# Kernel optimization log

Measured on AMD Instinct MI355X. Metric: run time of the kernel, lower is better.

## Reference

```python
import jax, jax.numpy as jnp
import numpy as np

N0, N1, N2 = 200000, 600000, 400000
NNZ1, NNZ2 = 1200000, 1200000
G = 256          # number of graphs in the batch
H = 128          # num_hidden
NIN = 32         # num_input
L = 2            # num_layers
R = 3            # max_rank + 1


def setup_inputs() -> dict:
    key = jax.random.key(0)
    ks = jax.random.split(key, 24)
    d = {}
    d["x0"] = jax.random.normal(ks[0], (N0, NIN), jnp.float32)
    d["x1"] = jax.random.normal(ks[1], (N1, NIN), jnp.float32)
    d["x2"] = jax.random.normal(ks[2], (N2, NIN), jnp.float32)
    d["b1_rows"] = jax.random.randint(ks[3], (NNZ1,), 0, N0, jnp.int32)
    d["b1_cols"] = jax.random.randint(ks[4], (NNZ1,), 0, N1, jnp.int32)
    d["b2_rows"] = jax.random.randint(ks[5], (NNZ2,), 0, N1, jnp.int32)
    d["b2_cols"] = jax.random.randint(ks[6], (NNZ2,), 0, N2, jnp.int32)
    d["batch0"] = jnp.sort(jax.random.randint(ks[7], (N0,), 0, G, jnp.int32))
    d["batch1"] = jnp.sort(jax.random.randint(ks[8], (N1,), 0, G, jnp.int32))
    d["batch2"] = jnp.sort(jax.random.randint(ks[9], (N2,), 0, G, jnp.int32))
    sin = 1.0 / np.sqrt(NIN).astype(np.float32)
    sh = 1.0 / np.sqrt(H).astype(np.float32)
    d["w_emb"] = jax.random.normal(ks[10], (NIN, H), jnp.float32) * sin
    d["b_emb"] = jnp.zeros((H,), jnp.float32)
    # one conv weight per (layer, rank>0): message W for B_r^T @ (x @ W)
    d["conv_w"] = jax.random.normal(ks[11], (L, 2, H, H), jnp.float32) * sh
    d["pre_w1"] = jax.random.normal(ks[12], (R, H, H), jnp.float32) * sh
    d["pre_b1"] = jnp.zeros((R, H), jnp.float32)
    d["pre_w2"] = jax.random.normal(ks[13], (R, H, H), jnp.float32) * sh
    d["pre_b2"] = jnp.zeros((R, H), jnp.float32)
    d["post_w1"] = jax.random.normal(ks[14], (R * H, H), jnp.float32) * (1.0 / np.sqrt(R * H).astype(np.float32))
    d["post_b1"] = jnp.zeros((H,), jnp.float32)
    d["post_w2"] = jax.random.normal(ks[15], (H, 1), jnp.float32) * sh
    d["post_b2"] = jnp.zeros((1,), jnp.float32)
    return d


def reference(x0, x1, x2, b1_rows, b1_cols, b2_rows, b2_cols,
              batch0, batch1, batch2,
              w_emb, b_emb, conv_w,
              pre_w1, pre_b1, pre_w2, pre_b2,
              post_w1, post_b1, post_w2, post_b2):
    # feature embedding (shared across ranks)
    h0 = x0 @ w_emb + b_emb
    h1 = x1 @ w_emb + b_emb
    h2 = x2 @ w_emb + b_emb

    for l in range(L):
        # sparse incidence matmul B_r^T @ h_{r-1}: gather rows, scatter-add to cols
        m1 = jax.ops.segment_sum(h0[b1_rows], b1_cols, num_segments=N1)
        m2 = jax.ops.segment_sum(h1[b2_rows], b2_cols, num_segments=N2)
        # aggregation with sigmoid update; rank 0 has no incoming messages
        h0 = jax.nn.sigmoid(h0)
        h1 = jax.nn.sigmoid(m1 @ conv_w[l, 0])
        h2 = jax.nn.sigmoid(m2 @ conv_w[l, 1])

    def pre_pool(h, r):
        z = jax.nn.silu(h @ pre_w1[r] + pre_b1[r])
        return z @ pre_w2[r] + pre_b2[r]

    # global_add_pool per rank -> [G, H] each
    p0 = jax.ops.segment_sum(pre_pool(h0, 0), batch0, num_segments=G)
    p1 = jax.ops.segment_sum(pre_pool(h1, 1), batch1, num_segments=G)
    p2 = jax.ops.segment_sum(pre_pool(h2, 2), batch2, num_segments=G)

    state = jnp.concatenate([p0, p1, p2], axis=1)  # [G, 3H]
    z = jax.nn.silu(state @ post_w1 + post_b1)
    out = z @ post_w2 + post_b2                     # [G, 1]
    return jnp.squeeze(out, axis=-1)                # [G]
```

## Files before the change

kernel.cpp:

```cpp
#include <hip/hip_runtime.h>
#include <math.h>

#define HDIM 128
#define NIN_ 32
#define RANKS 3

typedef unsigned int u32;
typedef unsigned short u16;
typedef __attribute__((ext_vector_type(8))) short short8;
typedef __attribute__((ext_vector_type(8))) __bf16 bf16x8;
typedef __attribute__((ext_vector_type(4))) float f32x4;

__device__ __forceinline__ u16 f2bf(float f) { return __builtin_bit_cast(u16, (__bf16)f); }
__device__ __forceinline__ float bf2f(u16 b) { return (float)__builtin_bit_cast(__bf16, b); }

__device__ __forceinline__ float sigmoidf_(float x) {
    return __builtin_amdgcn_rcpf(1.0f + __builtin_amdgcn_exp2f(-1.44269504f * x));
}
__device__ __forceinline__ float siluf_(float x) { return x * sigmoidf_(x); }

template <int SIG>
__device__ __forceinline__ float sigpow(float f) {
#pragma unroll
    for (int q = 0; q < SIG; ++q) f = sigmoidf_(f);
    return f;
}

__global__ void zero_kernel(u32* __restrict__ p, long long nw) {
    long long i = (long long)blockIdx.x * blockDim.x + threadIdx.x;
    long long stride = (long long)gridDim.x * blockDim.x;
    for (; i < nw; i += stride) p[i] = 0u;
}

__global__ void count2_kernel(const int* __restrict__ c1, int n1, int* __restrict__ cntA,
                              const int* __restrict__ c2, int n2, int* __restrict__ cntB) {
    int e = blockIdx.x * 256 + threadIdx.x;
    if (e < n1) atomicAdd(&cntA[c1[e]], 1);
    else if (e < n1 + n2) atomicAdd(&cntB[c2[e - n1]], 1);
}

__global__ void fill2_kernel(const int* __restrict__ r1, const int* __restrict__ c1,
                             int* __restrict__ curA, int* __restrict__ esrc1, int n1,
                             const int* __restrict__ r2, const int* __restrict__ c2,
                             int* __restrict__ curB, int* __restrict__ esrc2, int n2) {
    int e = blockIdx.x * 256 + threadIdx.x;
    if (e < n1) {
        int i = atomicAdd(&curA[c1[e]], 1);
        esrc1[i] = r1[e];
    } else if (e < n1 + n2) {
        int ee = e - n1;
        int i = atomicAdd(&curB[c2[ee]], 1);
        esrc2[i] = r2[ee];
    }
}

__global__ void scan1_kernel(const int* __restrict__ cnt, int* __restrict__ bsum, int ndst) {
    __shared__ int lds[256];
    int base = blockIdx.x * 1024, t = threadIdx.x;
    int s = 0;
#pragma unroll
    for (int j = 0; j < 4; ++j) {
        int i = base + t * 4 + j;
        s += (i < ndst) ? cnt[i] : 0;
    }
    lds[t] = s;
    __syncthreads();
    for (int off = 128; off > 0; off >>= 1) {
        if (t < off) lds[t] += lds[t + off];
        __syncthreads();
    }
    if (t == 0) bsum[blockIdx.x] = lds[0];
}

__global__ void scan2_kernel(int* __restrict__ bsum, int nb, int* __restrict__ total) {
    __shared__ int lds[256];
    int t = threadIdx.x;
    int v[8];
    int s = 0;
#pragma unroll
    for (int j = 0; j < 8; ++j) {
        int i = t * 8 + j;
        v[j] = (i < nb) ? bsum[i] : 0;
        s += v[j];
    }
    lds[t] = s;
    __syncthreads();
    for (int off = 1; off < 256; off <<= 1) {
        int y = (t >= off) ? lds[t - off] : 0;
        __syncthreads();
        lds[t] += y;
        __syncthreads();
    }
    int run = lds[t] - s;
#pragma unroll
    for (int j = 0; j < 8; ++j) {
        int i = t * 8 + j;
        if (i < nb) {
            bsum[i] = run;
            run += v[j];
        }
    }
    if (t == 255) *total = run;
}

__global__ void scan3_kernel(const int* __restrict__ cnt, const int* __restrict__ bsum,
                             int* __restrict__ rowptr, int* __restrict__ cursor, int ndst) {
    __shared__ int lds[256];
    int base = blockIdx.x * 1024, t = threadIdx.x;
    int v[4];
    int s = 0;
#pragma unroll
    for (int j = 0; j < 4; ++j) {
        int i = base + t * 4 + j;
        v[j] = (i < ndst) ? cnt[i] : 0;
        s += v[j];
    }
    lds[t] = s;
    __syncthreads();
    for (int off = 1; off < 256; off <<= 1) {
        int y = (t >= off) ? lds[t - off] : 0;
        __syncthreads();
        lds[t] += y;
        __syncthreads();
    }
    int run = bsum[blockIdx.x] + lds[t] - s;
#pragma unroll
    for (int j = 0; j < 4; ++j) {
        int i = base + t * 4 + j;
        if (i < ndst) {
            rowptr[i] = run;
            cursor[i] = run;
            run += v[j];
        }
    }
}

__global__ void wprep_kernel(const float* __restrict__ conv_w, const float* __restrict__ pre_w1,
                             const float* __restrict__ pre_w2, u16* __restrict__ wt, int Lnum) {
    int tid = blockIdx.x * 256 + threadIdx.x;
    int nm = 2 * Lnum + 6;
    if (tid >= nm * 128 * 128) return;
    int m = tid >> 14;
    int r = tid & 16383;
    int k = r >> 7;
    int col = r & 127;
    const float* src;
    if (m < 2 * Lnum) src = conv_w + (size_t)m * 16384;
    else if (m < 2 * Lnum + 3) src = pre_w1 + (size_t)(m - 2 * Lnum) * 16384;
    else src = pre_w2 + (size_t)(m - 2 * Lnum - 3) * 16384;
    float v = src[k * 128 + col];
    wt[(size_t)m * 16384 + col * 128 + (k ^ ((col & 7) << 3))] = f2bf(v);
}

__global__ void wembprep_kernel(const float* __restrict__ w_emb, u16* __restrict__ wembT) {
    int tid = blockIdx.x * 256 + threadIdx.x;
    if (tid >= HDIM * NIN_) return;
    int col = tid >> 5, k = tid & 31;
    wembT[col * 32 + k] = f2bf(w_emb[k * HDIM + col]);
}

__global__ __launch_bounds__(512) void embed_mfma_kernel(const float* __restrict__ x,
                                                         const u16* __restrict__ wembT,
                                                         const float* __restrict__ b,
                                                         u16* __restrict__ h, int n) {
    __shared__ u16 cs[8][16][128];
    const int tid = threadIdx.x;
    const int wave = tid >> 6, lane = tid & 63;
    const int row0 = blockIdx.x * 128;
    const int col = lane & 15, kg = lane >> 4;
    const int wrow0 = row0 + wave * 16;
    const int arow = wrow0 + col;
    const int arowc = arow < n ? arow : (n - 1);

    bf16x8 afrag;
    {
        const float4* xp = (const float4*)(x + (size_t)arowc * NIN_ + kg * 8);
        float4 xa = xp[0], xb = xp[1];
        short8 s;
        s[0] = (short)f2bf(xa.x); s[1] = (short)f2bf(xa.y);
        s[2] = (short)f2bf(xa.z); s[3] = (short)f2bf(xa.w);
        s[4] = (short)f2bf(xb.x); s[5] = (short)f2bf(xb.y);
        s[6] = (short)f2bf(xb.z); s[7] = (short)f2bf(xb.w);
        afrag = __builtin_bit_cast(bf16x8, s);
    }

#pragma unroll
    for (int ct = 0; ct < 8; ++ct) {
        int bcol = ct * 16 + col;
        bf16x8 bfrag = *(const bf16x8*)(wembT + bcol * 32 + kg * 8);
        f32x4 acc = (f32x4){0.f, 0.f, 0.f, 0.f};
        acc = __builtin_amdgcn_mfma_f32_16x16x32_bf16(afrag, bfrag, acc, 0, 0, 0);
        float bv = b[bcol];
#pragma unroll
        for (int r = 0; r < 4; ++r) {
            int crow = kg * 4 + r;
            cs[wave][crow][(ct * 16 + col) ^ ((crow & 7) << 3)] = f2bf(acc[r] + bv);
        }
    }
#pragma unroll
    for (int it = 0; it < 4; ++it) {
        int cid = it * 64 + lane;
        int r = cid >> 4, c = cid & 15;
        int grow = wrow0 + r;
        if (grow < n) {
            short8 v = *(const short8*)(&cs[wave][r][(c * 8) ^ ((r & 7) << 3)]);
            *(short8*)(h + (size_t)grow * HDIM + c * 8) = v;
        }
    }
}

__device__ __forceinline__ void gemm128(const bf16x8 afrag[4], const u16* wls, f32x4 acc[8],
                                        int col, int kg) {
#pragma unroll
    for (int ct = 0; ct < 8; ++ct) {
        int bcol = ct * 16 + col;
        const u16* bb = wls + bcol * 128;
        int swz = (bcol & 7) << 3;
#pragma unroll
        for (int k0 = 0; k0 < 4; ++k0) {
            bf16x8 bfrag = *(const bf16x8*)(bb + ((k0 * 32 + kg * 8) ^ swz));
            acc[ct] = __builtin_amdgcn_mfma_f32_16x16x32_bf16(afrag[k0], bfrag, acc[ct], 0, 0, 0);
        }
    }
}

__device__ __forceinline__ void stage_w(const u16* __restrict__ w, u16* wls, int tid) {
    const uint4* g = (const uint4*)w;
    uint4* l = (uint4*)wls;
#pragma unroll
    for (int i = 0; i < 4; ++i) l[tid + i * 512] = g[tid + i * 512];
}

__device__ __forceinline__ void pool_acc(const f32x4 acc[8], const float* __restrict__ b2,
                                         const int* __restrict__ batch, float* __restrict__ p,
                                         int n, int colOff, int wrow0, int col, int kg) {
    if (wrow0 >= n) return;
    int rend = wrow0 + 15 < n ? wrow0 + 15 : (n - 1);
    int bstart = batch[wrow0];
    int bend = batch[rend];
    if (bstart == bend) {
#pragma unroll
        for (int ct = 0; ct < 8; ++ct) {
            float b2v = b2[ct * 16 + col];
            float s = 0.f;
#pragma unroll
            for (int r = 0; r < 4; ++r) {
                int row = wrow0 + kg * 4 + r;
                if (row < n) s += acc[ct][r] + b2v;
            }
            s += __shfl_xor(s, 16, 64);
            s += __shfl_xor(s, 32, 64);
            if (kg == 0) atomicAdd(&p[bstart * (RANKS * HDIM) + colOff + ct * 16 + col], s);
        }
    } else {
        int bgs[4];
#pragma unroll
        for (int r = 0; r < 4; ++r) {
            int row = wrow0 + kg * 4 + r;
            bgs[r] = (row < n) ? batch[row] : -1;
        }
#pragma unroll
        for (int ct = 0; ct < 8; ++ct) {
            float b2v = b2[ct * 16 + col];
            int curb = -1;
            float cur = 0.f;
#pragma unroll
            for (int r = 0; r < 4; ++r) {
                if (bgs[r] >= 0) {
                    if (bgs[r] != curb) {
                        if (curb >= 0)
                            atomicAdd(&p[curb * (RANKS * HDIM) + colOff + ct * 16 + col], cur);
                        curb = bgs[r];
                        cur = 0.f;
                    }
                    cur += acc[ct][r] + b2v;
                }
            }
            if (curb >= 0) atomicAdd(&p[curb * (RANKS * HDIM) + colOff + ct * 16 + col], cur);
        }
    }
}

template <int SIGA>
__global__ __launch_bounds__(512) void merged_n1_kernel(
    const u16* __restrict__ srcbuf, const int* __restrict__ rowptr,
    const int* __restrict__ esrc, const u16* __restrict__ wc0, const u16* __restrict__ wc1,
    const u16* __restrict__ w1t, const u16* __restrict__ w2t,
    const float* __restrict__ b1, const float* __restrict__ b2,
    const int* __restrict__ batch, float* __restrict__ p, int colOff,
    u16* __restrict__ outB, int n) {
    __shared__ u16 wls[16384];
    __shared__ u16 zs[8][16][128];
    const int tid = threadIdx.x;
    const int wave = tid >> 6, lane = tid & 63;
    const int row0 = blockIdx.x * 128;
    const int col = lane & 15, kg = lane >> 4;
    const int wrow0 = row0 + wave * 16;

    stage_w(wc0, wls, tid);

    float gr[4][8], gs[4][8];
#pragma unroll
    for (int k0 = 0; k0 < 4; ++k0)
#pragma unroll
        for (int j = 0; j < 8; ++j) { gr[k0][j] = 0.f; gs[k0][j] = 0.f; }

    const int arow = wrow0 + col;
    if (arow < n) {
        int beg = rowptr[arow], end = rowptr[arow + 1];
        for (int e = beg; e < end; e += 2) {
            int s0 = esrc[e];
            bool has1 = (e + 1 < end);
            int s1 = has1 ? esrc[e + 1] : s0;
            const bf16x8* p0 = (const bf16x8*)(srcbuf + (size_t)s0 * HDIM + kg * 8);
            const bf16x8* p1 = (const bf16x8*)(srcbuf + (size_t)s1 * HDIM + kg * 8);
            bf16x8 v0[4], v1[4];
#pragma unroll
            for (int k0 = 0; k0 < 4; ++k0) { v0[k0] = p0[k0 * 4]; v1[k0] = p1[k0 * 4]; }
#pragma unroll
            for (int k0 = 0; k0 < 4; ++k0) {
                short8 sv = __builtin_bit_cast(short8, v0[k0]);
#pragma unroll
                for (int j = 0; j < 8; ++j) {
                    float f = sigpow<SIGA>(bf2f((u16)sv[j]));
                    gr[k0][j] += f;
                    gs[k0][j] += sigmoidf_(f);
                }
            }
            if (has1) {
#pragma unroll
                for (int k0 = 0; k0 < 4; ++k0) {
                    short8 sv = __builtin_bit_cast(short8, v1[k0]);
#pragma unroll
                    for (int j = 0; j < 8; ++j) {
                        float f = sigpow<SIGA>(bf2f((u16)sv[j]));
                        gr[k0][j] += f;
                        gs[k0][j] += sigmoidf_(f);
                    }
                }
            }
        }
    }
    bf16x8 afragR[4], afragS[4];
#pragma unroll
    for (int k0 = 0; k0 < 4; ++k0) {
        short8 sR, sS;
#pragma unroll
        for (int j = 0; j < 8; ++j) {
            sR[j] = (short)f2bf(gr[k0][j]);
            sS[j] = (short)f2bf(gs[k0][j]);
        }
        afragR[k0] = __builtin_bit_cast(bf16x8, sR);
        afragS[k0] = __builtin_bit_cast(bf16x8, sS);
    }
    __syncthreads();

    f32x4 acc[8];
#pragma unroll
    for (int ct = 0; ct < 8; ++ct) acc[ct] = (f32x4){0.f, 0.f, 0.f, 0.f};
    gemm128(afragR, wls, acc, col, kg);
#pragma unroll
    for (int ct = 0; ct < 8; ++ct)
#pragma unroll
        for (int r = 0; r < 4; ++r) {
            int crow = kg * 4 + r;
            zs[wave][crow][(ct * 16 + col) ^ ((crow & 7) << 3)] = f2bf(sigmoidf_(acc[ct][r]));
        }
#pragma unroll
    for (int it = 0; it < 4; ++it) {
        int cid = it * 64 + lane;
        int r = cid >> 4, c = cid & 15;
        int grow = wrow0 + r;
        if (grow < n) {
            short8 v = *(const short8*)(&zs[wave][r][(c * 8) ^ ((r & 7) << 3)]);
            *(short8*)(outB + (size_t)grow * HDIM + c * 8) = v;
        }
    }

    __syncthreads();
    stage_w(wc1, wls, tid);
    __syncthreads();

#pragma unroll
    for (int ct = 0; ct < 8; ++ct) acc[ct] = (f32x4){0.f, 0.f, 0.f, 0.f};
    gemm128(afragS, wls, acc, col, kg);
#pragma unroll
    for (int ct = 0; ct < 8; ++ct)
#pragma unroll
        for (int r = 0; r < 4; ++r) {
            int crow = kg * 4 + r;
            zs[wave][crow][(ct * 16 + col) ^ ((crow & 7) << 3)] = f2bf(sigmoidf_(acc[ct][r]));
        }
    __syncthreads();
    stage_w(w1t, wls, tid);
    __syncthreads();

    bf16x8 zfrag[4];
    {
        int zswz = (col & 7) << 3;
#pragma unroll
        for (int k0 = 0; k0 < 4; ++k0)
            zfrag[k0] = *(const bf16x8*)(&zs[wave][col][(k0 * 32 + kg * 8) ^ zswz]);
    }
#pragma unroll
    for (int ct = 0; ct < 8; ++ct) acc[ct] = (f32x4){0.f, 0.f, 0.f, 0.f};
    gemm128(zfrag, wls, acc, col, kg);
#pragma unroll
    for (int ct = 0; ct < 8; ++ct) {
        float b1v = b1[ct * 16 + col];
#pragma unroll
        for (int r = 0; r < 4; ++r) {
            int crow = kg * 4 + r;
            zs[wave][crow][(ct * 16 + col) ^ ((crow & 7) << 3)] = f2bf(siluf_(acc[ct][r] + b1v));
        }
    }
    __syncthreads();
    stage_w(w2t, wls, tid);
    __syncthreads();

    {
        int zswz = (col & 7) << 3;
#pragma unroll
        for (int k0 = 0; k0 < 4; ++k0)
            zfrag[k0] = *(const bf16x8*)(&zs[wave][col][(k0 * 32 + kg * 8) ^ zswz]);
    }
#pragma unroll
    for (int ct = 0; ct < 8; ++ct) acc[ct] = (f32x4){0.f, 0.f, 0.f, 0.f};
    gemm128(zfrag, wls, acc, col, kg);

    pool_acc(acc, b2, batch, p, n, colOff, wrow0, col, kg);
}

template <int MODE, int SIG>
__global__ __launch_bounds__(512) void fused_mfma_kernel(
    const u16* __restrict__ srcbuf, const int* __restrict__ rowptr,
    const int* __restrict__ esrc, const u16* __restrict__ wconv,
    const u16* __restrict__ w1t, const u16* __restrict__ w2t,
    const float* __restrict__ b1, const float* __restrict__ b2,
    const int* __restrict__ batch, float* __restrict__ p, int colOff,
    u16* __restrict__ outB, int n) {
    __shared__ u16 wls[16384];
    __shared__ u16 zs[8][16][128];
    const int tid = threadIdx.x;
    const int wave = tid >> 6, lane = tid & 63;
    const int row0 = blockIdx.x * 128;
    const int col = lane & 15, kg = lane >> 4;
    const int wrow0 = row0 + wave * 16;

    stage_w(wconv, wls, tid);

    float ga[4][8];
#pragma unroll
    for (int k0 = 0; k0 < 4; ++k0)
#pragma unroll
        for (int j = 0; j < 8; ++j) ga[k0][j] = 0.f;
    const int arow = wrow0 + col;
    if (arow < n) {
        int beg = rowptr[arow], end = rowptr[arow + 1];
        for (int e = beg; e < end; e += 2) {
            int s0 = esrc[e];
            bool has1 = (e + 1 < end);
            int s1 = has1 ? esrc[e + 1] : s0;
            const bf16x8* p0 = (const bf16x8*)(srcbuf + (size_t)s0 * HDIM + kg * 8);
            const bf16x8* p1 = (const bf16x8*)(srcbuf + (size_t)s1 * HDIM + kg * 8);
            bf16x8 v0[4], v1[4];
#pragma unroll
            for (int k0 = 0; k0 < 4; ++k0) { v0[k0] = p0[k0 * 4]; v1[k0] = p1[k0 * 4]; }
#pragma unroll
            for (int k0 = 0; k0 < 4; ++k0) {
                short8 sv = __builtin_bit_cast(short8, v0[k0]);
#pragma unroll
                for (int j = 0; j < 8; ++j) ga[k0][j] += sigpow<SIG>(bf2f((u16)sv[j]));
            }
            if (has1) {
#pragma unroll
                for (int k0 = 0; k0 < 4; ++k0) {
                    short8 sv = __builtin_bit_cast(short8, v1[k0]);
#pragma unroll
                    for (int j = 0; j < 8; ++j) ga[k0][j] += sigpow<SIG>(bf2f((u16)sv[j]));
                }
            }
        }
    }
    bf16x8 afrag[4];
#pragma unroll
    for (int k0 = 0; k0 < 4; ++k0) {
        short8 s;
#pragma unroll
        for (int j = 0; j < 8; ++j) s[j] = (short)f2bf(ga[k0][j]);
        afrag[k0] = __builtin_bit_cast(bf16x8, s);
    }
    __syncthreads();

    f32x4 acc[8];
#pragma unroll
    for (int ct = 0; ct < 8; ++ct) acc[ct] = (f32x4){0.f, 0.f, 0.f, 0.f};
    gemm128(afrag, wls, acc, col, kg);

#pragma unroll
    for (int ct = 0; ct < 8; ++ct)
#pragma unroll
        for (int r = 0; r < 4; ++r) {
            int crow = kg * 4 + r;
            zs[wave][crow][(ct * 16 + col) ^ ((crow & 7) << 3)] = f2bf(sigmoidf_(acc[ct][r]));
        }

    if (MODE == 0) {
#pragma unroll
        for (int it = 0; it < 4; ++it) {
            int cid = it * 64 + lane;
            int r = cid >> 4, c = cid & 15;
            int grow = wrow0 + r;
            if (grow < n) {
                short8 v = *(const short8*)(&zs[wave][r][(c * 8) ^ ((r & 7) << 3)]);
                *(short8*)(outB + (size_t)grow * HDIM + c * 8) = v;
            }
        }
        return;
    }

    __syncthreads();
    stage_w(w1t, wls, tid);
    __syncthreads();

    bf16x8 zfrag[4];
    {
        int zswz = (col & 7) << 3;
#pragma unroll
        for (int k0 = 0; k0 < 4; ++k0)
            zfrag[k0] = *(const bf16x8*)(&zs[wave][col][(k0 * 32 + kg * 8) ^ zswz]);
    }
#pragma unroll
    for (int ct = 0; ct < 8; ++ct) acc[ct] = (f32x4){0.f, 0.f, 0.f, 0.f};
    gemm128(zfrag, wls, acc, col, kg);
#pragma unroll
    for (int ct = 0; ct < 8; ++ct) {
        float b1v = b1[ct * 16 + col];
#pragma unroll
        for (int r = 0; r < 4; ++r) {
            int crow = kg * 4 + r;
            zs[wave][crow][(ct * 16 + col) ^ ((crow & 7) << 3)] = f2bf(siluf_(acc[ct][r] + b1v));
        }
    }
    __syncthreads();
    stage_w(w2t, wls, tid);
    __syncthreads();

    {
        int zswz = (col & 7) << 3;
#pragma unroll
        for (int k0 = 0; k0 < 4; ++k0)
            zfrag[k0] = *(const bf16x8*)(&zs[wave][col][(k0 * 32 + kg * 8) ^ zswz]);
    }
#pragma unroll
    for (int ct = 0; ct < 8; ++ct) acc[ct] = (f32x4){0.f, 0.f, 0.f, 0.f};
    gemm128(zfrag, wls, acc, col, kg);

    pool_acc(acc, b2, batch, p, n, colOff, wrow0, col, kg);
}

template <int SIG>
__global__ __launch_bounds__(512) void prepool_mfma_kernel(
    const u16* __restrict__ h, const u16* __restrict__ w1t, const u16* __restrict__ w2t,
    const float* __restrict__ b1, const float* __restrict__ b2, const int* __restrict__ batch,
    float* __restrict__ p, int n, int colOff) {
    __shared__ u16 wls[16384];
    __shared__ u16 zs[8][16][128];
    const int tid = threadIdx.x;
    const int wave = tid >> 6, lane = tid & 63;
    const int row0 = blockIdx.x * 128;
    const int col = lane & 15, kg = lane >> 4;
    const int wrow0 = row0 + wave * 16;

    stage_w(w1t, wls, tid);

    const int arow = wrow0 + col;
    const int arowc = arow < n ? arow : (n - 1);
    bf16x8 afrag[4];
    {
        const bf16x8* ap = (const bf16x8*)(h + (size_t)arowc * HDIM + kg * 8);
#pragma unroll
        for (int k0 = 0; k0 < 4; ++k0) afrag[k0] = ap[k0 * 4];
    }
    if (SIG > 0) {
#pragma unroll
        for (int k0 = 0; k0 < 4; ++k0) {
            short8 s = __builtin_bit_cast(short8, afrag[k0]);
#pragma unroll
            for (int j = 0; j < 8; ++j) s[j] = (short)f2bf(sigpow<SIG>(bf2f((u16)s[j])));
            afrag[k0] = __builtin_bit_cast(bf16x8, s);
        }
    }
    __syncthreads();

    f32x4 acc[8];
#pragma unroll
    for (int ct = 0; ct < 8; ++ct) acc[ct] = (f32x4){0.f, 0.f, 0.f, 0.f};
    gemm128(afrag, wls, acc, col, kg);
#pragma unroll
    for (int ct = 0; ct < 8; ++ct) {
        float b1v = b1[ct * 16 + col];
#pragma unroll
        for (int r = 0; r < 4; ++r) {
            int crow = kg * 4 + r;
            zs[wave][crow][(ct * 16 + col) ^ ((crow & 7) << 3)] = f2bf(siluf_(acc[ct][r] + b1v));
        }
    }
    __syncthreads();
    stage_w(w2t, wls, tid);
    __syncthreads();

    bf16x8 zfrag[4];
    {
        int zswz = (col & 7) << 3;
#pragma unroll
        for (int k0 = 0; k0 < 4; ++k0)
            zfrag[k0] = *(const bf16x8*)(&zs[wave][col][(k0 * 32 + kg * 8) ^ zswz]);
    }
#pragma unroll
    for (int ct = 0; ct < 8; ++ct) acc[ct] = (f32x4){0.f, 0.f, 0.f, 0.f};
    gemm128(zfrag, wls, acc, col, kg);

    pool_acc(acc, b2, batch, p, n, colOff, wrow0, col, kg);
}

__global__ void final_kernel(const float* __restrict__ p, const float* __restrict__ w1,
                             const float* __restrict__ b1, const float* __restrict__ w2,
                             const float* __restrict__ b2, float* __restrict__ out) {
    const int g = blockIdx.x;
    const int c = threadIdx.x;
    const float* pg = p + g * (RANKS * HDIM);
    float acc = b1[c];
    for (int k = 0; k < RANKS * HDIM; ++k) acc = fmaf(pg[k], w1[k * HDIM + c], acc);
    float z = siluf_(acc);
    float v = z * w2[c];
#pragma unroll
    for (int off = 32; off > 0; off >>= 1) v += __shfl_down(v, off, 64);
    __shared__ float red[2];
    if ((c & 63) == 0) red[c >> 6] = v;
    __syncthreads();
    if (c == 0) out[g] = red[0] + red[1] + b2[0];
}

extern "C" void kernel_launch(void* const* d_in, const int* in_sizes, int n_in,
                              void* d_out, int out_size, void* d_ws, size_t ws_size,
                              hipStream_t stream) {
    const float* x0 = (const float*)d_in[0];
    const float* x1 = (const float*)d_in[1];
    const int* b1_rows = (const int*)d_in[3];
    const int* b1_cols = (const int*)d_in[4];
    const int* b2_rows = (const int*)d_in[5];
    const int* b2_cols = (const int*)d_in[6];
    const int* batch0 = (const int*)d_in[7];
    const int* batch1 = (const int*)d_in[8];
    const int* batch2 = (const int*)d_in[9];
    const float* w_emb = (const float*)d_in[10];
    const float* b_emb = (const float*)d_in[11];
    const float* conv_w = (const float*)d_in[12];
    const float* pre_w1 = (const float*)d_in[13];
    const float* pre_b1 = (const float*)d_in[14];
    const float* pre_w2 = (const float*)d_in[15];
    const float* pre_b2 = (const float*)d_in[16];
    const float* post_w1 = (const float*)d_in[17];
    const float* post_b1 = (const float*)d_in[18];
    const float* post_w2 = (const float*)d_in[19];
    const float* post_b2 = (const float*)d_in[20];

    const int N0 = in_sizes[0] / NIN_;
    const int N1 = in_sizes[1] / NIN_;
    const int N2 = in_sizes[2] / NIN_;
    const int NNZ1 = in_sizes[3];
    const int NNZ2 = in_sizes[5];
    const int L = in_sizes[12] / (2 * HDIM * HDIM);
    const int Gn = out_size;

    u16* A = (u16*)d_ws;
    u16* B = A + (size_t)N0 * HDIM;
    float* p = (float*)(B + (size_t)N1 * HDIM);
    u16* wt = (u16*)(p + (size_t)Gn * RANKS * HDIM);
    const u16* wt_conv = wt;
    const u16* wt_p1 = wt + (size_t)2 * L * 16384;
    const u16* wt_p2 = wt_p1 + (size_t)3 * 16384;
    u16* wembT = wt + (size_t)(2 * L + 6) * 16384;
    int* ip = (int*)(wembT + 4096);
    int* rowptr1 = ip;  ip += N1 + 1;
    int* rowptr2 = ip;  ip += N2 + 1;
    int* esrc1 = ip;    ip += NNZ1;
    int* esrc2 = ip;    ip += NNZ2;
    int* cntA = ip;     ip += N1;
    int* cntB = ip;     ip += N2;
    int* curA = ip;     ip += N1;
    int* curB = ip;     ip += N2;
    int* bsum = ip;     ip += 2048;

    {
        int tot = (2 * L + 6) * 16384;
        wprep_kernel<<<(tot + 255) / 256, 256, 0, stream>>>(conv_w, pre_w1, pre_w2, wt, L);
        wembprep_kernel<<<16, 256, 0, stream>>>(w_emb, wembT);

        zero_kernel<<<1024, 256, 0, stream>>>((u32*)cntA, (long long)(N1 + N2));
        count2_kernel<<<(NNZ1 + NNZ2 + 255) / 256, 256, 0, stream>>>(b1_cols, NNZ1, cntA,
                                                                     b2_cols, NNZ2, cntB);
        int nb1 = (N1 + 1023) / 1024;
        scan1_kernel<<<nb1, 256, 0, stream>>>(cntA, bsum, N1);
        scan2_kernel<<<1, 256, 0, stream>>>(bsum, nb1, rowptr1 + N1);
        scan3_kernel<<<nb1, 256, 0, stream>>>(cntA, bsum, rowptr1, curA, N1);
        int nb2 = (N2 + 1023) / 1024;
        scan1_kernel<<<nb2, 256, 0, stream>>>(cntB, bsum, N2);
        scan2_kernel<<<1, 256, 0, stream>>>(bsum, nb2, rowptr2 + N2);
        scan3_kernel<<<nb2, 256, 0, stream>>>(cntB, bsum, rowptr2, curB, N2);
        fill2_kernel<<<(NNZ1 + NNZ2 + 255) / 256, 256, 0, stream>>>(
            b1_rows, b1_cols, curA, esrc1, NNZ1, b2_rows, b2_cols, curB, esrc2, NNZ2);
    }

    embed_mfma_kernel<<<(N0 + 127) / 128, 512, 0, stream>>>(x0, wembT, b_emb, A, N0);

    zero_kernel<<<64, 256, 0, stream>>>((u32*)p, (long long)Gn * RANKS * HDIM);

    if (L >= 2) {
        int grid = (N1 + 127) / 128;
        const u16* wc0 = wt_conv + (size_t)((L - 2) * 2 + 0) * 16384;
        const u16* wc1 = wt_conv + (size_t)((L - 1) * 2 + 0) * 16384;
        switch (L - 2) {
            case 0: merged_n1_kernel<0><<<grid, 512, 0, stream>>>(
                        A, rowptr1, esrc1, wc0, wc1, wt_p1 + 16384, wt_p2 + 16384,
                        pre_b1 + HDIM, pre_b2 + HDIM, batch1, p, HDIM, B, N1); break;
            case 1: merged_n1_kernel<1><<<grid, 512, 0, stream>>>(
                        A, rowptr1, esrc1, wc0, wc1, wt_p1 + 16384, wt_p2 + 16384,
                        pre_b1 + HDIM, pre_b2 + HDIM, batch1, p, HDIM, B, N1); break;
            default: merged_n1_kernel<2><<<grid, 512, 0, stream>>>(
                        A, rowptr1, esrc1, wc0, wc1, wt_p1 + 16384, wt_p2 + 16384,
                        pre_b1 + HDIM, pre_b2 + HDIM, batch1, p, HDIM, B, N1); break;
        }
    } else {
        embed_mfma_kernel<<<(N1 + 127) / 128, 512, 0, stream>>>(x1, wembT, b_emb, B, N1);
        fused_mfma_kernel<1, 0><<<(N1 + 127) / 128, 512, 0, stream>>>(
            A, rowptr1, esrc1, wt_conv, wt_p1 + 16384, wt_p2 + 16384,
            pre_b1 + HDIM, pre_b2 + HDIM, batch1, p, HDIM, nullptr, N1);
    }

    fused_mfma_kernel<1, 0><<<(N2 + 127) / 128, 512, 0, stream>>>(
        B, rowptr2, esrc2, wt_conv + (size_t)((L - 1) * 2 + 1) * 16384,
        wt_p1 + 2 * 16384, wt_p2 + 2 * 16384, pre_b1 + 2 * HDIM, pre_b2 + 2 * HDIM,
        batch2, p, 2 * HDIM, nullptr, N2);

    {
        int grid = (N0 + 127) / 128;
        switch (L) {
            case 1: prepool_mfma_kernel<1><<<grid, 512, 0, stream>>>(
                        A, wt_p1, wt_p2, pre_b1, pre_b2, batch0, p, N0, 0); break;
            case 2: prepool_mfma_kernel<2><<<grid, 512, 0, stream>>>(
                        A, wt_p1, wt_p2, pre_b1, pre_b2, batch0, p, N0, 0); break;
            default: prepool_mfma_kernel<3><<<grid, 512, 0, stream>>>(
                        A, wt_p1, wt_p2, pre_b1, pre_b2, batch0, p, N0, 0); break;
        }
    }

    final_kernel<<<Gn, HDIM, 0, stream>>>(p, post_w1, post_b1, post_w2, post_b2, (float*)d_out);
}
```

Baseline: 905.1 us.

## Read GEMM weights directly from global memory instead of staging in LDS

Removes the per-block LDS staging of 128x128 bf16 weight matrices and the barriers around it. The MFMA B fragments are now loaded straight from global or L2 memory, and the XOR swizzle is dropped from the weight layout. This cuts LDS use, which may raise occupancy, and removes the syncthreads stalls between GEMM stages. In exchange, every wave re-reads the weights through the cache hierarchy. The bf16 conversions are also replaced with manual bit-manipulation round-to-nearest-even code.

```diff
diff --git a/kernel.cpp b/kernel.cpp
--- a/kernel.cpp
+++ b/kernel.cpp
@@ -11,9 +11,12 @@
 typedef __attribute__((ext_vector_type(8))) __bf16 bf16x8;
 typedef __attribute__((ext_vector_type(4))) float f32x4;
 
-__device__ __forceinline__ u16 f2bf(float f) { return __builtin_bit_cast(u16, (__bf16)f); }
-__device__ __forceinline__ float bf2f(u16 b) { return (float)__builtin_bit_cast(__bf16, b); }
-
+__device__ __forceinline__ float bf2f(u16 b) { return __uint_as_float(((u32)b) << 16); }
+__device__ __forceinline__ u16 f2bf(float f) {
+    u32 u = __float_as_uint(f);
+    u32 r = u + 0x7fffu + ((u >> 16) & 1u);
+    return (u16)(r >> 16);
+}
 __device__ __forceinline__ float sigmoidf_(float x) {
     return __builtin_amdgcn_rcpf(1.0f + __builtin_amdgcn_exp2f(-1.44269504f * x));
 }
@@ -149,7 +152,7 @@
     else if (m < 2 * Lnum + 3) src = pre_w1 + (size_t)(m - 2 * Lnum) * 16384;
     else src = pre_w2 + (size_t)(m - 2 * Lnum - 3) * 16384;
     float v = src[k * 128 + col];
-    wt[(size_t)m * 16384 + col * 128 + (k ^ ((col & 7) << 3))] = f2bf(v);
+    wt[(size_t)m * 16384 + col * 128 + k] = f2bf(v);
 }
 
 __global__ void wembprep_kernel(const float* __restrict__ w_emb, u16* __restrict__ wembT) {
@@ -209,26 +212,18 @@
     }
 }
 
-__device__ __forceinline__ void gemm128(const bf16x8 afrag[4], const u16* wls, f32x4 acc[8],
-                                        int col, int kg) {
+__device__ __forceinline__ void gemm128g(const bf16x8 afrag[4], const u16* __restrict__ wt,
+                                         f32x4 acc[8], int col, int kg) {
 #pragma unroll
     for (int ct = 0; ct < 8; ++ct) {
         int bcol = ct * 16 + col;
-        const u16* bb = wls + bcol * 128;
-        int swz = (bcol & 7) << 3;
+        const u16* bb = wt + bcol * 128 + kg * 8;
 #pragma unroll
         for (int k0 = 0; k0 < 4; ++k0) {
-            bf16x8 bfrag = *(const bf16x8*)(bb + ((k0 * 32 + kg * 8) ^ swz));
+            bf16x8 bfrag = *(const bf16x8*)(bb + k0 * 32);
             acc[ct] = __builtin_amdgcn_mfma_f32_16x16x32_bf16(afrag[k0], bfrag, acc[ct], 0, 0, 0);
         }
     }
-}
-
-__device__ __forceinline__ void stage_w(const u16* __restrict__ w, u16* wls, int tid) {
-    const uint4* g = (const uint4*)w;
-    uint4* l = (uint4*)wls;
-#pragma unroll
-    for (int i = 0; i < 4; ++i) l[tid + i * 512] = g[tid + i * 512];
 }
 
 __device__ __forceinline__ void pool_acc(const f32x4 acc[8], const float* __restrict__ b2,
@@ -289,15 +284,12 @@
     const float* __restrict__ b1, const float* __restrict__ b2,
     const int* __restrict__ batch, float* __restrict__ p, int colOff,
     u16* __restrict__ outB, int n) {
-    __shared__ u16 wls[16384];
     __shared__ u16 zs[8][16][128];
     const int tid = threadIdx.x;
     const int wave = tid >> 6, lane = tid & 63;
     const int row0 = blockIdx.x * 128;
     const int col = lane & 15, kg = lane >> 4;
     const int wrow0 = row0 + wave * 16;
-
-    stage_w(wc0, wls, tid);
 
     float gr[4][8], gs[4][8];
 #pragma unroll
@@ -353,12 +345,11 @@
         afragR[k0] = __builtin_bit_cast(bf16x8, sR);
         afragS[k0] = __builtin_bit_cast(bf16x8, sS);
     }
-    __syncthreads();
 
     f32x4 acc[8];
 #pragma unroll
     for (int ct = 0; ct < 8; ++ct) acc[ct] = (f32x4){0.f, 0.f, 0.f, 0.f};
-    gemm128(afragR, wls, acc, col, kg);
+    gemm128g(afragR, wc0, acc, col, kg);
 #pragma unroll
     for (int ct = 0; ct < 8; ++ct)
 #pragma unroll
@@ -377,13 +368,9 @@
         }
     }
 
-    __syncthreads();
-    stage_w(wc1, wls, tid);
-    __syncthreads();
-
-#pragma unroll
-    for (int ct = 0; ct < 8; ++ct) acc[ct] = (f32x4){0.f, 0.f, 0.f, 0.f};
-    gemm128(afragS, wls, acc, col, kg);
+#pragma unroll
+    for (int ct = 0; ct < 8; ++ct) acc[ct] = (f32x4){0.f, 0.f, 0.f, 0.f};
+    gemm128g(afragS, wc1, acc, col, kg);
 #pragma unroll
     for (int ct = 0; ct < 8; ++ct)
 #pragma unroll
@@ -391,9 +378,6 @@
             int crow = kg * 4 + r;
             zs[wave][crow][(ct * 16 + col) ^ ((crow & 7) << 3)] = f2bf(sigmoidf_(acc[ct][r]));
         }
-    __syncthreads();
-    stage_w(w1t, wls, tid);
-    __syncthreads();
 
     bf16x8 zfrag[4];
     {
@@ -404,7 +388,7 @@
     }
 #pragma unroll
     for (int ct = 0; ct < 8; ++ct) acc[ct] = (f32x4){0.f, 0.f, 0.f, 0.f};
-    gemm128(zfrag, wls, acc, col, kg);
+    gemm128g(zfrag, w1t, acc, col, kg);
 #pragma unroll
     for (int ct = 0; ct < 8; ++ct) {
         float b1v = b1[ct * 16 + col];
@@ -414,9 +398,6 @@
             zs[wave][crow][(ct * 16 + col) ^ ((crow & 7) << 3)] = f2bf(siluf_(acc[ct][r] + b1v));
         }
     }
-    __syncthreads();
-    stage_w(w2t, wls, tid);
-    __syncthreads();
 
     {
         int zswz = (col & 7) << 3;
@@ -426,7 +407,7 @@
     }
 #pragma unroll
     for (int ct = 0; ct < 8; ++ct) acc[ct] = (f32x4){0.f, 0.f, 0.f, 0.f};
-    gemm128(zfrag, wls, acc, col, kg);
+    gemm128g(zfrag, w2t, acc, col, kg);
 
     pool_acc(acc, b2, batch, p, n, colOff, wrow0, col, kg);
 }
@@ -439,15 +420,12 @@
     const float* __restrict__ b1, const float* __restrict__ b2,
     const int* __restrict__ batch, float* __restrict__ p, int colOff,
     u16* __restrict__ outB, int n) {
-    __shared__ u16 wls[16384];
     __shared__ u16 zs[8][16][128];
     const int tid = threadIdx.x;
     const int wave = tid >> 6, lane = tid & 63;
     const int row0 = blockIdx.x * 128;
     const int col = lane & 15, kg = lane >> 4;
     const int wrow0 = row0 + wave * 16;
-
-    stage_w(wconv, wls, tid);
 
     float ga[4][8];
 #pragma unroll
@@ -490,12 +468,11 @@
         for (int j = 0; j < 8; ++j) s[j] = (short)f2bf(ga[k0][j]);
         afrag[k0] = __builtin_bit_cast(bf16x8, s);
     }
-    __syncthreads();
 
     f32x4 acc[8];
 #pragma unroll
     for (int ct = 0; ct < 8; ++ct) acc[ct] = (f32x4){0.f, 0.f, 0.f, 0.f};
-    gemm128(afrag, wls, acc, col, kg);
+    gemm128g(afrag, wconv, acc, col, kg);
 
 #pragma unroll
     for (int ct = 0; ct < 8; ++ct)
@@ -519,10 +496,6 @@
         return;
     }
 
-    __syncthreads();
-    stage_w(w1t, wls, tid);
-    __syncthreads();
-
     bf16x8 zfrag[4];
     {
         int zswz = (col & 7) << 3;
@@ -532,7 +505,7 @@
     }
 #pragma unroll
     for (int ct = 0; ct < 8; ++ct) acc[ct] = (f32x4){0.f, 0.f, 0.f, 0.f};
-    gemm128(zfrag, wls, acc, col, kg);
+    gemm128g(zfrag, w1t, acc, col, kg);
 #pragma unroll
     for (int ct = 0; ct < 8; ++ct) {
         float b1v = b1[ct * 16 + col];
@@ -542,9 +515,6 @@
             zs[wave][crow][(ct * 16 + col) ^ ((crow & 7) << 3)] = f2bf(siluf_(acc[ct][r] + b1v));
         }
     }
-    __syncthreads();
-    stage_w(w2t, wls, tid);
-    __syncthreads();
 
     {
         int zswz = (col & 7) << 3;
@@ -554,7 +524,7 @@
     }
 #pragma unroll
     for (int ct = 0; ct < 8; ++ct) acc[ct] = (f32x4){0.f, 0.f, 0.f, 0.f};
-    gemm128(zfrag, wls, acc, col, kg);
+    gemm128g(zfrag, w2t, acc, col, kg);
 
     pool_acc(acc, b2, batch, p, n, colOff, wrow0, col, kg);
 }
@@ -564,7 +534,6 @@
     const u16* __restrict__ h, const u16* __restrict__ w1t, const u16* __restrict__ w2t,
     const float* __restrict__ b1, const float* __restrict__ b2, const int* __restrict__ batch,
     float* __restrict__ p, int n, int colOff) {
-    __shared__ u16 wls[16384];
     __shared__ u16 zs[8][16][128];
     const int tid = threadIdx.x;
     const int wave = tid >> 6, lane = tid & 63;
@@ -572,8 +541,6 @@
     const int col = lane & 15, kg = lane >> 4;
     const int wrow0 = row0 + wave * 16;
 
-    stage_w(w1t, wls, tid);
-
     const int arow = wrow0 + col;
     const int arowc = arow < n ? arow : (n - 1);
     bf16x8 afrag[4];
@@ -591,12 +558,11 @@
             afrag[k0] = __builtin_bit_cast(bf16x8, s);
         }
     }
-    __syncthreads();
 
     f32x4 acc[8];
 #pragma unroll
     for (int ct = 0; ct < 8; ++ct) acc[ct] = (f32x4){0.f, 0.f, 0.f, 0.f};
-    gemm128(afrag, wls, acc, col, kg);
+    gemm128g(afrag, w1t, acc, col, kg);
 #pragma unroll
     for (int ct = 0; ct < 8; ++ct) {
         float b1v = b1[ct * 16 + col];
@@ -606,9 +572,6 @@
             zs[wave][crow][(ct * 16 + col) ^ ((crow & 7) << 3)] = f2bf(siluf_(acc[ct][r] + b1v));
         }
     }
-    __syncthreads();
-    stage_w(w2t, wls, tid);
-    __syncthreads();
 
     bf16x8 zfrag[4];
     {
@@ -619,7 +582,7 @@
     }
 #pragma unroll
     for (int ct = 0; ct < 8; ++ct) acc[ct] = (f32x4){0.f, 0.f, 0.f, 0.f};
-    gemm128(zfrag, wls, acc, col, kg);
+    gemm128g(zfrag, w2t, acc, col, kg);
 
     pool_acc(acc, b2, batch, p, n, colOff, wrow0, col, kg);
 }
```

After: 1.470 ms. 1.62x slower.
